# Performance work log

Hardware: AMD Instinct MI355X
Metric: run time of the kernel (lower is better)

The kernel has to match this reference:

```python
import jax, jax.numpy as jnp
import numpy as np

LAMB = 0.1
SIZE_AVERAGE = True


def setup_inputs() -> dict:
    key = jax.random.key(0)
    k1, k2 = jax.random.split(key)
    N, D = 8192, 4096
    inp = jax.random.normal(k1, (N, D), dtype=jnp.float32)
    target = jax.random.normal(k2, (N, D), dtype=jnp.float32)
    return {"input": inp, "target": target}


def _drae_loss(inp, target, lamb=LAMB, size_average=SIZE_AVERAGE):
    # Per-sample squared reconstruction error: Err[n] = sum_d (inp - target)^2
    err = (inp - target).reshape(inp.shape[0], -1)
    Err = jnp.sum(err * err, axis=1)                      # [N]
    N = Err.shape[0]
    sErr = jnp.sort(Err)                                  # ascending

    # Prefix sums replace the original O(N^2) Python scan.
    cs = jnp.cumsum(sErr)                                 # [N]
    cs2 = jnp.cumsum(sErr * sErr)                         # [N]
    total, total2 = cs[-1], cs2[-1]
    nf = jnp.asarray(N, sErr.dtype)
    allMean = total / nf
    Sb = total2 - nf * allMean * allMean                  # sum (e - allMean)^2

    # Candidate splits: inlier count k = 1..N-1 (loop index i = k-1).
    k = jnp.arange(1, N, dtype=sErr.dtype)                # [N-1]
    csk, cs2k = cs[:-1], cs2[:-1]
    Sw1 = cs2k - csk * csk / k                            # within-inlier scatter
    Sw2 = (total2 - cs2k) - (total - csk) ** 2 / (nf - k) # within-outlier scatter
    obj = (Sw1 + Sw2) / Sb                                # Fisher-style ratio

    i = jnp.argmin(obj)                                   # first min, like strict '<'
    optObj = obj[i]
    T = (i + 1).astype(sErr.dtype)                        # inlier count
    inlier_sum = cs[i]

    out = inlier_sum / T if size_average else inlier_sum
    return out + lamb * optObj


def reference(input, target):
    return _drae_loss(input, target)
```

## Files before the change

kernel.cpp:

```cpp
#include <hip/hip_runtime.h>

#define NROWS 8192
#define NCOLS 4096
#define LAMB  0.1
#define NBUCK 2048

typedef unsigned int u32;
typedef unsigned long long u64;

__global__ __launch_bounds__(256) void rowerr_kernel(const float* __restrict__ inp,
                                                     const float* __restrict__ tgt,
                                                     float* __restrict__ err) {
    const int row = blockIdx.x;
    const float4* a = reinterpret_cast<const float4*>(inp + (size_t)row * NCOLS);
    const float4* b = reinterpret_cast<const float4*>(tgt + (size_t)row * NCOLS);
    const int t = threadIdx.x;

    float acc = 0.f;
#pragma unroll
    for (int c = 0; c < 4; ++c) {
        float4 va = a[t + c * 256];
        float4 vb = b[t + c * 256];
        float dx = va.x - vb.x;
        float dy = va.y - vb.y;
        float dz = va.z - vb.z;
        float dw = va.w - vb.w;
        acc += dx * dx + dy * dy + dz * dz + dw * dw;
    }

#pragma unroll
    for (int off = 32; off > 0; off >>= 1) acc += __shfl_down(acc, off, 64);

    __shared__ float ws[4];
    const int lane = t & 63, wv = t >> 6;
    if (lane == 0) ws[wv] = acc;
    __syncthreads();
    if (t == 0) err[row] = ws[0] + ws[1] + ws[2] + ws[3];
}

__device__ __forceinline__ double fastrcp(double x) {
    double r = (double)(1.0f / (float)x);
    r = r * (2.0 - x * r);
    r = r * (2.0 - x * r);
    return r;
}

__global__ __launch_bounds__(1024) void drae_kernel(const float* __restrict__ err,
                                                    float* __restrict__ out) {
    const int N = NROWS;
    __shared__ u32 bufS[NROWS];
    __shared__ u32 bufB[NROWS];
    __shared__ u32 hist[NBUCK];
    __shared__ u32 base2[NBUCK];
    __shared__ u32 cnt2[NBUCK];
    __shared__ u32 sMin[16], sMax[16], saux[16];
    __shared__ double auxX[16], auxT2[16], redH[16], redCs[16];
    __shared__ int    redIdx[16];

    const int tid  = threadIdx.x;
    const int lane = tid & 63, wv = tid >> 6;

    u32 bits[8];
    u32 mn = 0xFFFFFFFFu, mx = 0u;
#pragma unroll
    for (int k = 0; k < 8; ++k) {
        bits[k] = __float_as_uint(err[tid + k * 1024]);
        mn = min(mn, bits[k]);
        mx = max(mx, bits[k]);
    }
#pragma unroll
    for (int off = 32; off > 0; off >>= 1) {
        mn = min(mn, (u32)__shfl_xor((int)mn, off, 64));
        mx = max(mx, (u32)__shfl_xor((int)mx, off, 64));
    }
    if (lane == 0) { sMin[wv] = mn; sMax[wv] = mx; }

    hist[tid] = 0;
    hist[tid + 1024] = 0;
    __syncthreads();

    u32 minb = sMin[0], maxb = sMax[0];
#pragma unroll
    for (int w = 1; w < 16; ++w) { minb = min(minb, sMin[w]); maxb = max(maxb, sMax[w]); }
    const u32 range = maxb - minb;
    const int nbits = 32 - __clz(range | 1u);
    const int shift = (nbits > 11) ? (nbits - 11) : 0;

    u32 bk[8];
#pragma unroll
    for (int k = 0; k < 8; ++k) {
        bits[k] -= minb;
        bk[k] = bits[k] >> shift;
        atomicAdd(&hist[bk[k]], 1u);
    }
    __syncthreads();

    const u32 c0 = hist[2 * tid], c1 = hist[2 * tid + 1];
    const u32 tsum = c0 + c1;
    u32 incl = tsum;
#pragma unroll
    for (int off = 1; off < 64; off <<= 1) {
        const u32 t = __shfl_up(incl, off, 64);
        if (lane >= off) incl += t;
    }
    if (lane == 63) saux[wv] = incl;
    __syncthreads();
    u32 add = 0;
#pragma unroll
    for (int w = 0; w < 16; ++w) if (w < wv) add += saux[w];
    const u32 excl = add + incl - tsum;
    base2[2 * tid] = excl;           base2[2 * tid + 1] = excl + c0;
    cnt2[2 * tid]  = c0;             cnt2[2 * tid + 1]  = c1;
    hist[2 * tid]  = excl;           hist[2 * tid + 1]  = excl + c0;
    __syncthreads();

    u32 myq[8];
#pragma unroll
    for (int k = 0; k < 8; ++k) {
        const u32 p = atomicAdd(&hist[bk[k]], 1u);
        myq[k] = p - base2[bk[k]];
        bufB[p] = bits[k];
    }
    __syncthreads();

#pragma unroll
    for (int k = 0; k < 8; ++k) {
        const u32 s = base2[bk[k]];
        const u32 c = cnt2[bk[k]];
        const u32 ki = bits[k];
        u32 r = 0;
        for (u32 q = 0; q < c; ++q) {
            const u32 v = bufB[s + q];
            r += (v < ki || (v == ki && q < myq[k])) ? 1u : 0u;
        }
        bufS[s + r] = ki;
    }
    __syncthreads();

    float v[8];
#pragma unroll
    for (int r = 0; r < 8; ++r) v[r] = __uint_as_float(bufS[(tid << 3) + r] + minb);

    double sx = 0.0, sx2 = 0.0;
#pragma unroll
    for (int r = 0; r < 8; ++r) {
        sx  += (double)v[r];
        sx2 += (double)v[r] * (double)v[r];
    }

    double ix = sx;
#pragma unroll
    for (int off = 1; off < 64; off <<= 1) {
        double t1 = __shfl_up(ix, off, 64);
        if (lane >= off) ix += t1;
    }
    double t2 = sx2;
#pragma unroll
    for (int off = 32; off > 0; off >>= 1) t2 += __shfl_xor(t2, off, 64);

    if (lane == 63) auxX[wv]  = ix;
    if (lane == 0)  auxT2[wv] = t2;
    __syncthreads();

    double wOff1 = 0.0, total1 = 0.0, total2 = 0.0;
#pragma unroll
    for (int w = 0; w < 16; ++w) {
        const double a1 = auxX[w];
        if (w < wv) wOff1 += a1;
        total1 += a1;
        total2 += auxT2[w];
    }
    const double exc1 = wOff1 + (ix - sx);
    const double nf = (double)N;

    double run1 = exc1;
    double bestH = -1e300, bestCs = 0.0;
    int bestIdx = N;
#pragma unroll
    for (int r = 0; r < 8; ++r) {
        const int idx = (tid << 3) + r;
        run1 += (double)v[r];
        if (idx < N - 1) {
            const double kf  = (double)(idx + 1);
            const double rem = total1 - run1;
            const double h   = run1 * run1 * fastrcp(kf) +
                               rem  * rem  * fastrcp(nf - kf);
            if (h > bestH) { bestH = h; bestIdx = idx; bestCs = run1; }
        }
    }

#pragma unroll
    for (int off = 32; off > 0; off >>= 1) {
        const double oH   = __shfl_down(bestH, off, 64);
        const int    oIdx = __shfl_down(bestIdx, off, 64);
        const double oCs  = __shfl_down(bestCs, off, 64);
        if (oH > bestH || (oH == bestH && oIdx < bestIdx)) {
            bestH = oH; bestIdx = oIdx; bestCs = oCs;
        }
    }
    if (lane == 0) { redH[wv] = bestH; redIdx[wv] = bestIdx; redCs[wv] = bestCs; }
    __syncthreads();

    if (tid == 0) {
        double bH = redH[0], bCs = redCs[0];
        int bIdx = redIdx[0];
        for (int w = 1; w < 16; ++w) {
            if (redH[w] > bH || (redH[w] == bH && redIdx[w] < bIdx)) {
                bH = redH[w]; bIdx = redIdx[w]; bCs = redCs[w];
            }
        }
        const double Sb     = total2 - total1 * total1 / nf;
        const double optObj = (total2 - bH) / Sb;
        const double T      = (double)(bIdx + 1);
        out[0] = (float)(bCs / T + LAMB * optObj);
    }
}

extern "C" void kernel_launch(void* const* d_in, const int* in_sizes, int n_in,
                              void* d_out, int out_size, void* d_ws, size_t ws_size,
                              hipStream_t stream) {
    const float* inp = (const float*)d_in[0];
    const float* tgt = (const float*)d_in[1];
    float* errbuf = (float*)d_ws;

    rowerr_kernel<<<NROWS, 256, 0, stream>>>(inp, tgt, errbuf);
    drae_kernel<<<1, 1024, 0, stream>>>(errbuf, (float*)d_out);
}
```

Measured before the change: 67.06 us.

## Fuse min/max into row-error kernel and trim shared buffers in sort kernel

The row-error kernel now folds each row's error bits into a global min/max with atomics, so the single-block sort kernel no longer runs its own min/max reduction and barrier. The sort kernel loads errors as float4, derives bucket counts from the post-scatter hist instead of a separate cnt2 array, and reuses bufB for the sorted output instead of a separate bufS, cutting shared memory. In exchange it adds two memset calls per launch and 16K global atomics on two addresses. The load order now differs from the original layout, but sorting does not depend on it.

```diff
diff --git a/kernel.cpp b/kernel.cpp
--- a/kernel.cpp
+++ b/kernel.cpp
@@ -10,7 +10,8 @@
 
 __global__ __launch_bounds__(256) void rowerr_kernel(const float* __restrict__ inp,
                                                      const float* __restrict__ tgt,
-                                                     float* __restrict__ err) {
+                                                     float* __restrict__ err,
+                                                     u32* __restrict__ minmax) {
     const int row = blockIdx.x;
     const float4* a = reinterpret_cast<const float4*>(inp + (size_t)row * NCOLS);
     const float4* b = reinterpret_cast<const float4*>(tgt + (size_t)row * NCOLS);
@@ -35,7 +36,13 @@
     const int lane = t & 63, wv = t >> 6;
     if (lane == 0) ws[wv] = acc;
     __syncthreads();
-    if (t == 0) err[row] = ws[0] + ws[1] + ws[2] + ws[3];
+    if (t == 0) {
+        const float v = ws[0] + ws[1] + ws[2] + ws[3];
+        err[row] = v;
+        const u32 bits = __float_as_uint(v);
+        atomicMin(&minmax[0], bits);
+        atomicMax(&minmax[1], bits);
+    }
 }
 
 __device__ __forceinline__ double fastrcp(double x) {
@@ -46,53 +53,50 @@
 }
 
 __global__ __launch_bounds__(1024) void drae_kernel(const float* __restrict__ err,
+                                                    const u32* __restrict__ minmax,
                                                     float* __restrict__ out) {
     const int N = NROWS;
-    __shared__ u32 bufS[NROWS];
     __shared__ u32 bufB[NROWS];
     __shared__ u32 hist[NBUCK];
     __shared__ u32 base2[NBUCK];
-    __shared__ u32 cnt2[NBUCK];
-    __shared__ u32 sMin[16], sMax[16], saux[16];
+    __shared__ u32 saux[16];
     __shared__ double auxX[16], auxT2[16], redH[16], redCs[16];
     __shared__ int    redIdx[16];
 
     const int tid  = threadIdx.x;
     const int lane = tid & 63, wv = tid >> 6;
 
-    u32 bits[8];
-    u32 mn = 0xFFFFFFFFu, mx = 0u;
-#pragma unroll
-    for (int k = 0; k < 8; ++k) {
-        bits[k] = __float_as_uint(err[tid + k * 1024]);
-        mn = min(mn, bits[k]);
-        mx = max(mx, bits[k]);
-    }
-#pragma unroll
-    for (int off = 32; off > 0; off >>= 1) {
-        mn = min(mn, (u32)__shfl_xor((int)mn, off, 64));
-        mx = max(mx, (u32)__shfl_xor((int)mx, off, 64));
-    }
-    if (lane == 0) { sMin[wv] = mn; sMax[wv] = mx; }
-
     hist[tid] = 0;
     hist[tid + 1024] = 0;
-    __syncthreads();
-
-    u32 minb = sMin[0], maxb = sMax[0];
-#pragma unroll
-    for (int w = 1; w < 16; ++w) { minb = min(minb, sMin[w]); maxb = max(maxb, sMax[w]); }
+
+    const u32 minb = minmax[0];
+    const u32 maxb = minmax[1];
     const u32 range = maxb - minb;
     const int nbits = 32 - __clz(range | 1u);
     const int shift = (nbits > 11) ? (nbits - 11) : 0;
 
+    u32 bits[8];
+    {
+        const float4* e4 = reinterpret_cast<const float4*>(err);
+        const float4 f0 = e4[tid];
+        const float4 f1 = e4[tid + 1024];
+        bits[0] = __float_as_uint(f0.x) - minb;
+        bits[1] = __float_as_uint(f0.y) - minb;
+        bits[2] = __float_as_uint(f0.z) - minb;
+        bits[3] = __float_as_uint(f0.w) - minb;
+        bits[4] = __float_as_uint(f1.x) - minb;
+        bits[5] = __float_as_uint(f1.y) - minb;
+        bits[6] = __float_as_uint(f1.z) - minb;
+        bits[7] = __float_as_uint(f1.w) - minb;
+    }
     u32 bk[8];
 #pragma unroll
-    for (int k = 0; k < 8; ++k) {
-        bits[k] -= minb;
-        bk[k] = bits[k] >> shift;
-        atomicAdd(&hist[bk[k]], 1u);
-    }
+    for (int k = 0; k < 8; ++k) bk[k] = bits[k] >> shift;
+
+    __syncthreads();
+
+#pragma unroll
+    for (int k = 0; k < 8; ++k) atomicAdd(&hist[bk[k]], 1u);
     __syncthreads();
 
     const u32 c0 = hist[2 * tid], c1 = hist[2 * tid + 1];
@@ -110,7 +114,6 @@
     for (int w = 0; w < 16; ++w) if (w < wv) add += saux[w];
     const u32 excl = add + incl - tsum;
     base2[2 * tid] = excl;           base2[2 * tid + 1] = excl + c0;
-    cnt2[2 * tid]  = c0;             cnt2[2 * tid + 1]  = c1;
     hist[2 * tid]  = excl;           hist[2 * tid + 1]  = excl + c0;
     __syncthreads();
 
@@ -123,23 +126,28 @@
     }
     __syncthreads();
 
+    u32 pos[8];
 #pragma unroll
     for (int k = 0; k < 8; ++k) {
         const u32 s = base2[bk[k]];
-        const u32 c = cnt2[bk[k]];
+        const u32 e = hist[bk[k]];
         const u32 ki = bits[k];
         u32 r = 0;
-        for (u32 q = 0; q < c; ++q) {
+        for (u32 q = 0; q < e - s; ++q) {
             const u32 v = bufB[s + q];
             r += (v < ki || (v == ki && q < myq[k])) ? 1u : 0u;
         }
-        bufS[s + r] = ki;
-    }
+        pos[k] = s + r;
+    }
+    __syncthreads();
+
+#pragma unroll
+    for (int k = 0; k < 8; ++k) bufB[pos[k]] = bits[k];
     __syncthreads();
 
     float v[8];
 #pragma unroll
-    for (int r = 0; r < 8; ++r) v[r] = __uint_as_float(bufS[(tid << 3) + r] + minb);
+    for (int r = 0; r < 8; ++r) v[r] = __uint_as_float(bufB[(tid << 3) + r] + minb);
 
     double sx = 0.0, sx2 = 0.0;
 #pragma unroll
@@ -222,7 +230,10 @@
     const float* inp = (const float*)d_in[0];
     const float* tgt = (const float*)d_in[1];
     float* errbuf = (float*)d_ws;
-
-    rowerr_kernel<<<NROWS, 256, 0, stream>>>(inp, tgt, errbuf);
-    drae_kernel<<<1, 1024, 0, stream>>>(errbuf, (float*)d_out);
-}
+    u32*   minmax = (u32*)((char*)d_ws + NROWS * 4);
+
+    hipMemsetAsync(&minmax[0], 0xFF, 4, stream);
+    hipMemsetAsync(&minmax[1], 0x00, 4, stream);
+    rowerr_kernel<<<NROWS, 256, 0, stream>>>(inp, tgt, errbuf, minmax);
+    drae_kernel<<<1, 1024, 0, stream>>>(errbuf, minmax, (float*)d_out);
+}
```

Result: slower. 228.0 us (+240.0%).
